# Kernel tuning notes

Hardware: AMD Instinct MI355X
Metric: run time of the kernel (lower is better)

## Reference

```python
import jax, jax.numpy as jnp
import numpy as np

NC = 80          # num classes
REG_MAX = 16     # DFL bins
STRIDES = (8, 16, 32)
FEAT_HW = ((80, 80), (40, 40), (20, 20))
MAX_DET = 100
CONF_THRES = 0.25
IOU_THRES = 0.45
PRE_TOPK = 1000  # pre-NMS candidate count (EfficientNMS-style preselection)


def setup_inputs() -> dict:
    key = jax.random.key(0)
    k1, k2, k3 = jax.random.split(key, 3)
    B = 32
    no = 4 * REG_MAX + NC  # 144
    return {
        "p3": jax.random.normal(k1, (B, no, 80, 80), dtype=jnp.float32),
        "p4": jax.random.normal(k2, (B, no, 40, 40), dtype=jnp.float32),
        "p5": jax.random.normal(k3, (B, no, 20, 20), dtype=jnp.float32),
    }


def _make_anchors():
    # grid_cell_offset = 0.5, matching ultralytics make_anchors
    pts, strs = [], []
    for (h, w), s in zip(FEAT_HW, STRIDES):
        sx = jnp.arange(w, dtype=jnp.float32) + 0.5
        sy = jnp.arange(h, dtype=jnp.float32) + 0.5
        yy, xx = jnp.meshgrid(sy, sx, indexing="ij")
        pts.append(jnp.stack([xx.ravel(), yy.ravel()], axis=-1))  # [h*w, 2]
        strs.append(jnp.full((h * w, 1), float(s), dtype=jnp.float32))
    return jnp.concatenate(pts, 0), jnp.concatenate(strs, 0)  # [A,2], [A,1]


def _pairwise_iou(b):
    # b: [K, 4] xyxy
    area = (b[:, 2] - b[:, 0]) * (b[:, 3] - b[:, 1])
    lt = jnp.maximum(b[:, None, :2], b[None, :, :2])
    rb = jnp.minimum(b[:, None, 2:], b[None, :, 2:])
    wh = jnp.clip(rb - lt, 0.0)
    inter = wh[..., 0] * wh[..., 1]
    return inter / (area[:, None] + area[None, :] - inter + 1e-7)


def _nms_single(bxyxy, conf):
    # Greedy class-agnostic NMS over PRE_TOPK score-sorted boxes.
    K = bxyxy.shape[0]
    iou = _pairwise_iou(bxyxy)  # [K, K]
    idx = jnp.arange(K)

    def step(suppressed, xs):
        i, row = xs
        keep = jnp.logical_and(jnp.logical_not(suppressed[i]), conf[i] > 0.0)
        suppressed = jnp.logical_or(suppressed, keep & (row > IOU_THRES) & (idx > i))
        return suppressed, keep

    _, keeps = jax.lax.scan(step, jnp.zeros(K, dtype=bool), (idx, iou))
    return keeps  # [K] bool


def reference(p3, p4, p5):
    feats = [p3, p4, p5]
    B = p3.shape[0]
    no = 4 * REG_MAX + NC
    # concat across scales: [B, no, A]
    x_cat = jnp.concatenate([f.reshape(B, no, -1) for f in feats], axis=2)
    box, cls = x_cat[:, : 4 * REG_MAX], x_cat[:, 4 * REG_MAX:]

    anchors, strd = _make_anchors()  # [A,2], [A,1]
    A = box.shape[-1]

    # DFL: softmax over reg_max bins, expectation with arange weights
    prob = jax.nn.softmax(box.reshape(B, 4, REG_MAX, A), axis=2)
    dist = jnp.einsum("bkra,r->bka", prob, jnp.arange(REG_MAX, dtype=jnp.float32))

    # dist2bbox (xywh) then scale by stride
    anc = anchors.T  # [2, A]
    lt, rb = dist[:, :2], dist[:, 2:]
    x1y1 = anc - lt
    x2y2 = anc + rb
    dbox = jnp.concatenate([(x1y1 + x2y2) * 0.5, x2y2 - x1y1], axis=1) * strd.T  # [B,4,A]

    boxes = dbox.transpose(0, 2, 1)                       # [B, A, 4] xywh
    scores = jax.nn.sigmoid(cls).transpose(0, 2, 1)       # [B, A, NC] (score_activation=1)

    # class-agnostic: best class per box
    conf = scores.max(-1)                                 # [B, A]
    cls_id = jnp.argmax(scores, -1)                       # [B, A]
    conf_m = jnp.where(conf > CONF_THRES, conf, -1.0)

    topv, topi = jax.lax.top_k(conf_m, PRE_TOPK)          # [B, K]
    bsel = jnp.take_along_axis(boxes, topi[..., None], axis=1)  # [B, K, 4]
    cx, cy, w, h = bsel[..., 0], bsel[..., 1], bsel[..., 2], bsel[..., 3]
    bxyxy = jnp.stack([cx - w * 0.5, cy - h * 0.5, cx + w * 0.5, cy + h * 0.5], -1)

    keeps = jax.vmap(_nms_single)(bxyxy, topv)            # [B, K]
    kept_scores = jnp.where(keeps, topv, -1.0)
    dv, di = jax.lax.top_k(kept_scores, MAX_DET)          # [B, MAX_DET]
    valid = dv > 0.0

    det_scores = jnp.where(valid, dv, 0.0)
    det_boxes = jnp.take_along_axis(bxyxy, di[..., None], axis=1) * valid[..., None]
    sel_cls = jnp.take_along_axis(jnp.take_along_axis(cls_id, topi, 1), di, 1)
    det_classes = jnp.where(valid, sel_cls, 0).astype(jnp.int32)
    num_dets = valid.sum(-1, keepdims=True).astype(jnp.int32)
    return num_dets, det_boxes, det_scores, det_classes
```

## Files before the change

kernel.cpp:

```cpp
#include <hip/hip_runtime.h>
#include <math.h>

#define NCLS 80
#define NA 8400
#define NB 32
#define NO 144
#define PRE_TOPK 1000
#define MAX_DET 100

template<int HW, int WDIM, int S>
__device__ __forceinline__ void decode_store(
    const float* __restrict__ src, int g, int aoff,
    float* __restrict__ conf, int* __restrict__ clsid, float* __restrict__ box)
{
    int b = g / HW;
    int pos = g - b * HW;
    float ax = (float)(pos % WDIM) + 0.5f;
    float ay = (float)(pos / WDIM) + 0.5f;
    const float* base = src + (size_t)b * (NO * HW) + pos;

    float dist[4];
    #pragma unroll
    for (int s4 = 0; s4 < 4; ++s4) {
        float v[16];
        #pragma unroll
        for (int r = 0; r < 16; ++r) v[r] = base[(size_t)(s4 * 16 + r) * HW];
        float mm = v[0];
        #pragma unroll
        for (int r = 1; r < 16; ++r) mm = fmaxf(mm, v[r]);
        float sum = 0.f;
        #pragma unroll
        for (int r = 0; r < 16; ++r) { v[r] = __expf(v[r] - mm); sum += v[r]; }
        float inv = 1.0f / sum;
        float d = 0.f;
        #pragma unroll
        for (int r = 1; r < 16; ++r) d += (v[r] * inv) * (float)r;
        dist[s4] = d;
    }

    float best = -INFINITY; int bid = 0;
    #pragma unroll
    for (int ch = 0; ch < 4; ++ch) {
        float vc[20];
        #pragma unroll
        for (int c = 0; c < 20; ++c) vc[c] = base[(size_t)(64 + ch * 20 + c) * HW];
        float m = vc[0]; int ii = 0;
        #pragma unroll
        for (int c = 1; c < 20; ++c) if (vc[c] > m) { m = vc[c]; ii = c; }
        if (m > best) { best = m; bid = ch * 20 + ii; }
    }
    float conf_v = 1.0f / (1.0f + __expf(-best));

    float x1 = ax - dist[0], y1 = ay - dist[1];
    float x2 = ax + dist[2], y2 = ay + dist[3];
    float cx = ((x1 + x2) * 0.5f) * (float)S;
    float cy = ((y1 + y2) * 0.5f) * (float)S;
    float w  = (x2 - x1) * (float)S;
    float h  = (y2 - y1) * (float)S;

    size_t gid = (size_t)b * NA + aoff + pos;
    conf[gid]  = conf_v;
    clsid[gid] = bid;
    *(float4*)(box + gid * 4) = make_float4(cx, cy, w, h);
}

__global__ __launch_bounds__(256) void k_decode(
    const float* __restrict__ p3, const float* __restrict__ p4, const float* __restrict__ p5,
    float* __restrict__ conf, int* __restrict__ clsid, float* __restrict__ box)
{
    int blk = blockIdx.x;
    int t = threadIdx.x;
    if (blk < 800) {
        int g = blk * 256 + t;
        decode_store<6400, 80, 8>(p3, g, 0, conf, clsid, box);
    } else if (blk < 1000) {
        int g = (blk - 800) * 256 + t;
        decode_store<1600, 40, 16>(p4, g, 6400, conf, clsid, box);
    } else {
        int g = (blk - 1000) * 256 + t;
        decode_store<400, 20, 32>(p5, g, 8000, conf, clsid, box);
    }
}

__device__ __forceinline__ uint32_t ord_bits(float f) {
    uint32_t u = __float_as_uint(f);
    return (u & 0x80000000u) ? ~u : (u | 0x80000000u);
}

__global__ __launch_bounds__(1024) void k_select(
    const float* __restrict__ conf, const float* __restrict__ box, const int* __restrict__ clsid,
    float* __restrict__ topv, float* __restrict__ bxyxy, int* __restrict__ topcls)
{
    int b = blockIdx.x;
    int t = threadIdx.x;
    int lane = t & 63;

    __shared__ uint32_t ob[NA];
    __shared__ uint32_t hist[256];
    __shared__ uint64_t sbuf[1024];
    __shared__ uint64_t s_prefix;
    __shared__ int s_k;
    __shared__ int s_cnt;

    const float* cf = conf + (size_t)b * NA;
    for (int i = t; i < NA; i += 1024) {
        float c = cf[i];
        float cm = (c > 0.25f) ? c : -1.0f;
        ob[i] = ord_bits(cm);
    }
    if (t == 0) { s_prefix = 0; s_k = PRE_TOPK; s_cnt = 0; }
    sbuf[t] = 0;
    __syncthreads();

    for (int pass = 0; pass < 8; ++pass) {
        int shift = 56 - 8 * pass;
        if (t < 256) hist[t] = 0;
        __syncthreads();
        uint64_t prefix = s_prefix;
        int k = s_k;
        for (int i = t; i < NA; i += 1024) {
            uint64_t key = ((uint64_t)ob[i] << 32) | (uint64_t)(0xFFFFFFFFu - (uint32_t)i);
            bool match = (pass == 0) || (((key ^ prefix) >> (64 - 8 * pass)) == 0);
            uint32_t d = (uint32_t)(key >> shift) & 255u;
            if (match) {
                uint64_t m = __ballot(1);
                #pragma unroll
                for (int bb = 0; bb < 8; ++bb) {
                    uint64_t bal = __ballot((d >> bb) & 1u);
                    m &= ((d >> bb) & 1u) ? bal : ~bal;
                }
                if ((m & ((1ull << lane) - 1ull)) == 0ull)
                    atomicAdd(&hist[d], (uint32_t)__popcll(m));
            }
        }
        __syncthreads();
        if (t < 64) {
            uint32_t h0 = hist[4 * t + 0], h1 = hist[4 * t + 1];
            uint32_t h2 = hist[4 * t + 2], h3 = hist[4 * t + 3];
            uint32_t part = h0 + h1 + h2 + h3;
            uint32_t s = part;
            #pragma unroll
            for (int off = 1; off < 64; off <<= 1) {
                uint32_t v = __shfl_down(s, off);
                if (t + off < 64) s += v;
            }
            uint32_t cb3 = s - part;
            uint32_t cb2 = cb3 + h3;
            uint32_t cb1 = cb2 + h2;
            uint32_t cb0 = cb1 + h1;
            uint32_t ku = (uint32_t)k;
            if (cb3 < ku && ku <= cb3 + h3) { s_k = k - (int)cb3; s_prefix = prefix | ((uint64_t)(uint32_t)(4 * t + 3) << shift); }
            if (cb2 < ku && ku <= cb2 + h2) { s_k = k - (int)cb2; s_prefix = prefix | ((uint64_t)(uint32_t)(4 * t + 2) << shift); }
            if (cb1 < ku && ku <= cb1 + h1) { s_k = k - (int)cb1; s_prefix = prefix | ((uint64_t)(uint32_t)(4 * t + 1) << shift); }
            if (cb0 < ku && ku <= cb0 + h0) { s_k = k - (int)cb0; s_prefix = prefix | ((uint64_t)(uint32_t)(4 * t + 0) << shift); }
        }
        __syncthreads();
    }

    uint64_t kstar = s_prefix;
    for (int i = t; i < NA; i += 1024) {
        uint64_t key = ((uint64_t)ob[i] << 32) | (uint64_t)(0xFFFFFFFFu - (uint32_t)i);
        if (key >= kstar) {
            int p = atomicAdd(&s_cnt, 1);
            if (p < 1024) sbuf[p] = key;
        }
    }
    __syncthreads();

    for (int k = 2; k <= 1024; k <<= 1) {
        for (int j = k >> 1; j > 0; j >>= 1) {
            int ixj = t ^ j;
            if (ixj > t) {
                uint64_t A = sbuf[t], Bv = sbuf[ixj];
                bool descBlock = ((t & k) == 0);
                bool sw = descBlock ? (A < Bv) : (A > Bv);
                if (sw) { sbuf[t] = Bv; sbuf[ixj] = A; }
            }
            __syncthreads();
        }
    }

    if (t < PRE_TOPK) {
        uint64_t key = sbuf[t];
        uint32_t u = (uint32_t)(key >> 32);
        uint32_t fb = (u & 0x80000000u) ? (u ^ 0x80000000u) : ~u;
        float val = __uint_as_float(fb);
        int idx = (int)(0xFFFFFFFFu - (uint32_t)(key & 0xFFFFFFFFull));
        size_t g = (size_t)b * NA + idx;
        float4 bx = *(const float4*)(box + g * 4);
        float cx = bx.x, cy = bx.y, w = bx.z, h = bx.w;
        size_t o = (size_t)b * PRE_TOPK + t;
        topv[o] = val;
        *(float4*)(bxyxy + o * 4) = make_float4(cx - w * 0.5f, cy - h * 0.5f,
                                                cx + w * 0.5f, cy + h * 0.5f);
        topcls[o] = clsid[g];
    }
}

__device__ __forceinline__ int bslot(int j) { return j + (j >> 6); }

__global__ __launch_bounds__(256) void k_iou(
    const float* __restrict__ bxyxy, unsigned long long* __restrict__ mask)
{
    __shared__ float4 boxes[PRE_TOPK + 16];
    int b = blockIdx.y;
    int t = threadIdx.x;
    const float4* bp = (const float4*)(bxyxy + (size_t)b * PRE_TOPK * 4);
    for (int i = t; i < PRE_TOPK; i += 256) boxes[bslot(i)] = bp[i];
    __syncthreads();

    int r_local = t >> 4, w = t & 15;
    int row = blockIdx.x * 16 + r_local;
    if (row >= PRE_TOPK) return;

    float4 bi = boxes[bslot(row)];
    float area_i = (bi.z - bi.x) * (bi.w - bi.y);
    unsigned long long bits = 0;
    int j0 = w * 64;
    #pragma unroll 4
    for (int jj = 0; jj < 64; ++jj) {
        int j = j0 + jj;
        if (j >= PRE_TOPK) break;
        if (j <= row) continue;
        float4 bj = boxes[bslot(j)];
        float lx = fmaxf(bi.x, bj.x), ly = fmaxf(bi.y, bj.y);
        float rx = fminf(bi.z, bj.z), ry = fminf(bi.w, bj.w);
        float iw = fmaxf(rx - lx, 0.f), ih = fmaxf(ry - ly, 0.f);
        float inter = iw * ih;
        float area_j = (bj.z - bj.x) * (bj.w - bj.y);
        float iou = inter / (area_i + area_j - inter + 1e-7f);
        if (iou > 0.45f) bits |= (1ull << jj);
    }
    mask[((size_t)b * PRE_TOPK + row) * 16 + w] = bits;
}

__global__ __launch_bounds__(1024) void k_nms(
    const unsigned long long* __restrict__ mask, const float* __restrict__ topv,
    const float* __restrict__ bxyxy, const int* __restrict__ topcls,
    float* __restrict__ out)
{
    int b = blockIdx.x;
    int t = threadIdx.x;

    __shared__ __align__(16) unsigned long long smask[PRE_TOPK * 16];
    __shared__ float sv[PRE_TOPK];
    __shared__ unsigned long long s_valid[16];
    __shared__ int kept[MAX_DET];
    __shared__ int s_cnt;

    for (int i = t; i < PRE_TOPK; i += 1024) sv[i] = topv[(size_t)b * PRE_TOPK + i];
    {
        const ulonglong2* src = (const ulonglong2*)(mask + (size_t)b * PRE_TOPK * 16);
        ulonglong2* dst = (ulonglong2*)smask;
        for (int i = t; i < PRE_TOPK * 8; i += 1024) dst[i] = src[i];
    }
    __syncthreads();

    {
        bool pred = (t < PRE_TOPK) && (sv[t] > 0.0f);
        unsigned long long bal = __ballot(pred);
        if ((t & 63) == 0) s_valid[t >> 6] = bal;
    }
    __syncthreads();

    if (t < 64) {
        int w = t;
        unsigned long long supp = 0;
        unsigned long long valid = (w < 16) ? s_valid[w] : 0ull;
        int base = w * 64;
        int cur = -1;
        int cnt = 0;
        while (cnt < MAX_DET) {
            unsigned long long gt;
            if (cur < base)            gt = ~0ull;
            else if (cur - base >= 63) gt = 0ull;
            else                       gt = (~0ull) << (cur - base + 1);
            unsigned long long cand = valid & ~supp & gt;
            int idx = cand ? (base + __builtin_ctzll(cand)) : 0x7FFFFFFF;
            #pragma unroll
            for (int off = 8; off >= 1; off >>= 1) {
                int o = __shfl_xor(idx, off);
                idx = (o < idx) ? o : idx;
            }
            int nxt = __shfl(idx, 0);
            if (nxt == 0x7FFFFFFF) break;
            if (t == 0) kept[cnt] = nxt;
            ++cnt;
            if (w < 16) supp |= smask[nxt * 16 + w];
            cur = nxt;
        }
        if (t == 0) s_cnt = cnt;
    }
    __syncthreads();

    int cnt = s_cnt; if (cnt > MAX_DET) cnt = MAX_DET;
    if (t == 0) out[b] = (float)cnt;
    if (t < MAX_DET) {
        bool valid = t < cnt;
        float bx0 = 0.f, bx1 = 0.f, bx2 = 0.f, bx3 = 0.f, sc = 0.f, cl = 0.f;
        if (valid) {
            int p = kept[t];
            size_t o = (size_t)b * PRE_TOPK + p;
            float4 bb = *(const float4*)(bxyxy + o * 4);
            bx0 = bb.x; bx1 = bb.y; bx2 = bb.z; bx3 = bb.w;
            sc = sv[p];
            cl = (float)topcls[o];
        }
        size_t db = 32 + ((size_t)b * MAX_DET + t) * 4;
        out[db + 0] = bx0; out[db + 1] = bx1; out[db + 2] = bx2; out[db + 3] = bx3;
        out[32 + 12800 + (size_t)b * MAX_DET + t] = sc;
        out[32 + 16000 + (size_t)b * MAX_DET + t] = cl;
    }
}

extern "C" void kernel_launch(void* const* d_in, const int* in_sizes, int n_in,
                              void* d_out, int out_size, void* d_ws, size_t ws_size,
                              hipStream_t stream)
{
    const float* p3 = (const float*)d_in[0];
    const float* p4 = (const float*)d_in[1];
    const float* p5 = (const float*)d_in[2];
    float* out = (float*)d_out;

    char* ws = (char*)d_ws;
    size_t off_mask = 0;
    size_t off_conf = off_mask + (size_t)NB * PRE_TOPK * 16 * 8;
    size_t off_cls  = off_conf + (size_t)NB * NA * 4;
    size_t off_box  = off_cls  + (size_t)NB * NA * 4;
    size_t off_topv = off_box  + (size_t)NB * NA * 4 * 4;
    size_t off_topc = off_topv + (size_t)NB * PRE_TOPK * 4;
    size_t off_bx   = off_topc + (size_t)NB * PRE_TOPK * 4;

    unsigned long long* mask = (unsigned long long*)(ws + off_mask);
    float* conf   = (float*)(ws + off_conf);
    int*   clsid  = (int*)(ws + off_cls);
    float* box    = (float*)(ws + off_box);
    float* topv   = (float*)(ws + off_topv);
    int*   topcls = (int*)(ws + off_topc);
    float* bxyxy  = (float*)(ws + off_bx);

    k_decode<<<1050, 256, 0, stream>>>(p3, p4, p5, conf, clsid, box);
    k_select<<<NB, 1024, 0, stream>>>(conf, box, clsid, topv, bxyxy, topcls);
    k_iou<<<dim3((PRE_TOPK + 15) / 16, NB), 256, 0, stream>>>(bxyxy, mask);
    k_nms<<<NB, 1024, 0, stream>>>(mask, topv, bxyxy, topcls, out);
}
```

Measured before the change: 144.2 us.

## Batch decode loads, fuse DFL normalize, and use register bitonic sort with shuffles

The decode kernel now issues all 64 box-bin loads up front and interleaves the class-logit loads with the DFL softmax math, so more loads are in flight at once. DFL folds the normalization into a single multiply, and launch bounds request 4 blocks per SM. The top-k bitonic sort keeps each key in a register and exchanges partners with wavefront shuffles for distances below 64, using shared memory only for larger strides. The cost is higher register pressure in decode, which the occupancy hint may force into spills.

```diff
diff --git a/kernel.cpp b/kernel.cpp
--- a/kernel.cpp
+++ b/kernel.cpp
@@ -8,6 +8,27 @@
 #define PRE_TOPK 1000
 #define MAX_DET 100
 
+__device__ __forceinline__ float dfl16(const float* v) {
+    float mm = v[0];
+    #pragma unroll
+    for (int r = 1; r < 16; ++r) mm = fmaxf(mm, v[r]);
+    float sum = 0.f, d = 0.f;
+    #pragma unroll
+    for (int r = 0; r < 16; ++r) {
+        float e = __expf(v[r] - mm);
+        sum += e;
+        d += e * (float)r;
+    }
+    return d * (1.0f / sum);
+}
+
+__device__ __forceinline__ void cls20(const float* v, int chbase, float& best, int& bid) {
+    float m = v[0]; int ii = 0;
+    #pragma unroll
+    for (int c = 1; c < 20; ++c) if (v[c] > m) { m = v[c]; ii = c; }
+    if (m > best) { best = m; bid = chbase + ii; }
+}
+
 template<int HW, int WDIM, int S>
 __device__ __forceinline__ void decode_store(
     const float* __restrict__ src, int g, int aoff,
@@ -19,40 +40,39 @@
     float ay = (float)(pos / WDIM) + 0.5f;
     const float* base = src + (size_t)b * (NO * HW) + pos;
 
-    float dist[4];
-    #pragma unroll
-    for (int s4 = 0; s4 < 4; ++s4) {
-        float v[16];
-        #pragma unroll
-        for (int r = 0; r < 16; ++r) v[r] = base[(size_t)(s4 * 16 + r) * HW];
-        float mm = v[0];
-        #pragma unroll
-        for (int r = 1; r < 16; ++r) mm = fmaxf(mm, v[r]);
-        float sum = 0.f;
-        #pragma unroll
-        for (int r = 0; r < 16; ++r) { v[r] = __expf(v[r] - mm); sum += v[r]; }
-        float inv = 1.0f / sum;
-        float d = 0.f;
-        #pragma unroll
-        for (int r = 1; r < 16; ++r) d += (v[r] * inv) * (float)r;
-        dist[s4] = d;
-    }
-
+    float g0[16], g1[16], g2[16], g3[16];
+    float c0[20], c1[20], c2[20], c3[20];
+
+    #pragma unroll
+    for (int r = 0; r < 16; ++r) g0[r] = base[(size_t)r * HW];
+    #pragma unroll
+    for (int r = 0; r < 16; ++r) g1[r] = base[(size_t)(16 + r) * HW];
+    #pragma unroll
+    for (int r = 0; r < 16; ++r) g2[r] = base[(size_t)(32 + r) * HW];
+    #pragma unroll
+    for (int r = 0; r < 16; ++r) g3[r] = base[(size_t)(48 + r) * HW];
+    float d0 = dfl16(g0);
+    float d1 = dfl16(g1);
+    #pragma unroll
+    for (int c = 0; c < 20; ++c) c0[c] = base[(size_t)(64 + c) * HW];
+    #pragma unroll
+    for (int c = 0; c < 20; ++c) c1[c] = base[(size_t)(84 + c) * HW];
+    float d2 = dfl16(g2);
+    float d3 = dfl16(g3);
+    #pragma unroll
+    for (int c = 0; c < 20; ++c) c2[c] = base[(size_t)(104 + c) * HW];
+    #pragma unroll
+    for (int c = 0; c < 20; ++c) c3[c] = base[(size_t)(124 + c) * HW];
     float best = -INFINITY; int bid = 0;
-    #pragma unroll
-    for (int ch = 0; ch < 4; ++ch) {
-        float vc[20];
-        #pragma unroll
-        for (int c = 0; c < 20; ++c) vc[c] = base[(size_t)(64 + ch * 20 + c) * HW];
-        float m = vc[0]; int ii = 0;
-        #pragma unroll
-        for (int c = 1; c < 20; ++c) if (vc[c] > m) { m = vc[c]; ii = c; }
-        if (m > best) { best = m; bid = ch * 20 + ii; }
-    }
+    cls20(c0, 0, best, bid);
+    cls20(c1, 20, best, bid);
+    cls20(c2, 40, best, bid);
+    cls20(c3, 60, best, bid);
+
     float conf_v = 1.0f / (1.0f + __expf(-best));
 
-    float x1 = ax - dist[0], y1 = ay - dist[1];
-    float x2 = ax + dist[2], y2 = ay + dist[3];
+    float x1 = ax - d0, y1 = ay - d1;
+    float x2 = ax + d2, y2 = ay + d3;
     float cx = ((x1 + x2) * 0.5f) * (float)S;
     float cy = ((y1 + y2) * 0.5f) * (float)S;
     float w  = (x2 - x1) * (float)S;
@@ -64,7 +84,7 @@
     *(float4*)(box + gid * 4) = make_float4(cx, cy, w, h);
 }
 
-__global__ __launch_bounds__(256) void k_decode(
+__global__ __launch_bounds__(256, 4) void k_decode(
     const float* __restrict__ p3, const float* __restrict__ p4, const float* __restrict__ p5,
     float* __restrict__ conf, int* __restrict__ clsid, float* __restrict__ box)
 {
@@ -167,21 +187,26 @@
     }
     __syncthreads();
 
+    uint64_t v = sbuf[t];
     for (int k = 2; k <= 1024; k <<= 1) {
         for (int j = k >> 1; j > 0; j >>= 1) {
-            int ixj = t ^ j;
-            if (ixj > t) {
-                uint64_t A = sbuf[t], Bv = sbuf[ixj];
-                bool descBlock = ((t & k) == 0);
-                bool sw = descBlock ? (A < Bv) : (A > Bv);
-                if (sw) { sbuf[t] = Bv; sbuf[ixj] = A; }
+            uint64_t o;
+            if (j >= 64) {
+                sbuf[t] = v;
+                __syncthreads();
+                o = sbuf[t ^ j];
+                __syncthreads();
+            } else {
+                o = __shfl_xor((unsigned long long)v, j);
             }
-            __syncthreads();
+            bool desc  = ((t & k) == 0);
+            bool lower = ((t & j) == 0);
+            v = (desc == lower) ? (v > o ? v : o) : (v < o ? v : o);
         }
     }
 
     if (t < PRE_TOPK) {
-        uint64_t key = sbuf[t];
+        uint64_t key = v;
         uint32_t u = (uint32_t)(key >> 32);
         uint32_t fb = (u & 0x80000000u) ? (u ^ 0x80000000u) : ~u;
         float val = __uint_as_float(fb);
```

New measurement: 154.7 us. 1.07x slower.
